# Kernel tuning notes

Measured on AMD Instinct MI355X. Metric: run time of the kernel, lower is better.

The kernel has to match this reference:

```python
import jax, jax.numpy as jnp
import numpy as np

EPS = 1e-7
K = 15      # kernel_size
CIN = 128
F = 256


def setup_inputs() -> dict:
    key = jax.random.key(0)
    k1, k2 = jax.random.split(key)
    x = jax.random.normal(k1, (32, 4096, CIN), dtype=jnp.float32)
    # glorot-uniform init then UnitNorm over axes (0,1) per filter, matching the constraint
    limit = np.sqrt(6.0 / (K * CIN + F))
    kernel = jax.random.uniform(k2, (K, CIN, F), dtype=jnp.float32, minval=-limit, maxval=limit)
    kernel = kernel / jnp.sqrt(jnp.sum(kernel * kernel, axis=(0, 1), keepdims=True) + 1e-12)
    scale = jnp.full((1, 1, 1), 10.0, dtype=jnp.float32)
    bias = jnp.zeros((F,), dtype=jnp.float32)
    return {"inputs": x, "kernel": kernel, "scale": scale, "bias": bias}


def reference(inputs, kernel, scale, bias):
    # dot-product conv: (B, L-K+1, F), VALID padding, stride 1
    dot = jax.lax.conv_general_dilated(
        inputs, kernel, window_strides=(1,), padding="VALID",
        dimension_numbers=("NWC", "WIO", "NWC"))
    # sliding sum-of-squares over window*channels. In the original this is a
    # conv1d with an all-ones (K,CIN,F) kernel, i.e. every filter sees the same
    # scalar sum -> compute it once via a cumsum box filter and broadcast.
    k = kernel.shape[0]
    sq = jnp.sum(inputs * inputs, axis=-1)                       # (B, L)
    cs = jnp.cumsum(jnp.pad(sq, ((0, 0), (1, 0))), axis=1)       # (B, L+1)
    win = cs[:, k:] - cs[:, :-k]                                 # (B, L-K+1)
    norm_x = jnp.sqrt(win + EPS)[..., None]                      # (B, L-K+1, 1)
    return scale * (dot / norm_x) + bias
```

## Files before the change

kernel.cpp:

```cpp
#include <hip/hip_runtime.h>
#include <hip/hip_bf16.h>
#include <stdint.h>

#define K_TAPS 15
#define CIN    128
#define F_OUT  256
#define LSEQ   4096
#define LOUT   (LSEQ - K_TAPS + 1)
#define BATCH  32

typedef __attribute__((ext_vector_type(8))) short bf16x8;
typedef __attribute__((ext_vector_type(4))) float f32x4;

typedef __attribute__((address_space(1))) const unsigned int gu32_t;
typedef __attribute__((address_space(3))) unsigned int su32_t;

__global__ void prep_w_kernel(const float* __restrict__ W,
                              unsigned short* __restrict__ Wp) {
  int idx = blockIdx.x * 256 + threadIdx.x;
  int f  = idx & 255;
  int kc = idx >> 8;
  int c  = kc & 127;
  int k  = kc >> 7;
  float w = W[idx];
  __hip_bfloat16 hb = __float2bfloat16(w);
  int chalf = c >> 6;
  int c6    = c & 63;
  int slot  = ((c6 >> 3) ^ f) & 7;
  int cp    = slot * 8 + (c & 7);
  Wp[((size_t)(k * 2 + chalf) * 256 + f) * 64 + cp] =
      *reinterpret_cast<unsigned short*>(&hb);
}

__global__ void sq_kernel(const float* __restrict__ x, float* __restrict__ sq) {
  int wid  = threadIdx.x >> 6;
  int lane = threadIdx.x & 63;
  int half = lane >> 5;
  int lq   = lane & 31;
  long pos = (long)blockIdx.x * 8 + wid * 2 + half;
  const float4* xp = (const float4*)(x + pos * CIN) + lq;
  float4 v = *xp;
  float s = v.x * v.x + v.y * v.y + v.z * v.z + v.w * v.w;
  #pragma unroll
  for (int m = 1; m <= 16; m <<= 1) s += __shfl_xor(s, m, 64);
  if (lq == 0) sq[pos] = s;
}

__global__ void rn_kernel(const float* __restrict__ sq,
                          const float* __restrict__ scale,
                          float* __restrict__ rn) {
  int t = blockIdx.x * 256 + threadIdx.x;
  int b = blockIdx.y;
  if (t >= LOUT) return;
  const float* s = sq + b * LSEQ + t;
  float w = 0.f;
  #pragma unroll
  for (int k = 0; k < K_TAPS; ++k) w += s[k];
  rn[b * LSEQ + t] = scale[0] / sqrtf(w + 1e-7f);
}

#define BM 256
#define BN 256
#define XROWS 272
#define XBYTES (XROWS * 256)
#define BBYTES 32768
#define NSTEP (K_TAPS * 2)

__global__ __launch_bounds__(512, 2) void conv_gemm_kernel(
    const float* __restrict__ x, const unsigned short* __restrict__ Wp,
    const float* __restrict__ rn, const float* __restrict__ bias,
    float* __restrict__ out)
{
  __shared__ __align__(16) char lds[XBYTES + 2 * BBYTES];
  char* Xs = lds;
  char* Bs = lds + XBYTES;

  const int b  = blockIdx.y;
  const int t0 = blockIdx.x * BM;

  const int tx   = threadIdx.x;
  const int wid  = tx >> 6;
  const int lane = tx & 63;
  const int wm   = wid >> 2;
  const int wn   = wid & 3;

  const int klane = lane >> 4;
  const int rl    = lane & 15;
  const int arow0 = wm * 128;
  const int bcol0 = wn * 64;

  auto stageB = [&](int buf, int step) {
    const char* src = (const char*)Wp + (size_t)step * 32768;
    char* dst = Bs + buf * BBYTES;
    #pragma unroll
    for (int i = 0; i < 4; ++i) {
      int off = i * 8192 + wid * 1024;
      __builtin_amdgcn_global_load_lds(
          (gu32_t*)(src + off + lane * 16),
          (su32_t*)(dst + off), 16, 0, 0);
    }
  };

  stageB(0, 0);

  {
    const int rloc = tx >> 4;
    const int g    = tx & 15;
    const float* xb = x + (long)b * LSEQ * CIN;
    #pragma unroll
    for (int it = 0; it < 9; ++it) {
      int row  = it * 32 + rloc;
      int grow = t0 + row;
      if (row < XROWS) {
        float v[8];
        if (grow < LSEQ) {
          const float4* p = (const float4*)(xb + (long)grow * CIN + g * 8);
          float4 a0 = p[0], a1 = p[1];
          v[0]=a0.x; v[1]=a0.y; v[2]=a0.z; v[3]=a0.w;
          v[4]=a1.x; v[5]=a1.y; v[6]=a1.z; v[7]=a1.w;
        } else {
          #pragma unroll
          for (int j = 0; j < 8; ++j) v[j] = 0.f;
        }
        union { unsigned short us[8]; int4 q; } pk;
        #pragma unroll
        for (int j = 0; j < 8; ++j) {
          __hip_bfloat16 hb = __float2bfloat16(v[j]);
          pk.us[j] = *reinterpret_cast<unsigned short*>(&hb);
        }
        int slot = (g & 8) | ((g ^ row) & 7);
        *(int4*)(Xs + row * 256 + slot * 16) = pk.q;
      }
    }
  }
  __syncthreads();

  f32x4 acc[8][4] = {};

  #pragma unroll 2
  for (int s = 0; s < NSTEP; ++s) {
    const int tap = s >> 1;
    const int ch8 = (s & 1) * 8;
    const char* Bsc = Bs + (s & 1) * BBYTES;

    bf16x8 afA[4], afB[4], bfr0[4], bfr1[4];

    {
      const int ga = ch8 + klane;
      #pragma unroll
      for (int i = 0; i < 4; ++i) {
        int row  = arow0 + i * 16 + rl + tap;
        int slot = (ga & 8) | ((ga ^ row) & 7);
        afA[i] = *(const bf16x8*)(Xs + row * 256 + slot * 16);
      }
      #pragma unroll
      for (int nf = 0; nf < 4; ++nf) {
        int fc   = bcol0 + nf * 16 + rl;
        int slot = (klane ^ fc) & 7;
        bfr0[nf] = *(const bf16x8*)(Bsc + fc * 128 + slot * 16);
      }
      if (s + 1 < NSTEP) stageB((s & 1) ^ 1, s + 1);
    }
    __builtin_amdgcn_s_barrier();
    asm volatile("s_waitcnt lgkmcnt(0)" ::: "memory");
    __builtin_amdgcn_s_setprio(1);
    #pragma unroll
    for (int i = 0; i < 4; ++i)
      #pragma unroll
      for (int nf = 0; nf < 4; ++nf)
        acc[i][nf] = __builtin_amdgcn_mfma_f32_16x16x32_bf16(
            afA[i], bfr0[nf], acc[i][nf], 0, 0, 0);
    __builtin_amdgcn_s_setprio(0);
    __builtin_amdgcn_s_barrier();

    {
      const int ga = ch8 + klane;
      #pragma unroll
      for (int i = 0; i < 4; ++i) {
        int row  = arow0 + (i + 4) * 16 + rl + tap;
        int slot = (ga & 8) | ((ga ^ row) & 7);
        afB[i] = *(const bf16x8*)(Xs + row * 256 + slot * 16);
      }
    }
    __builtin_amdgcn_s_barrier();
    asm volatile("s_waitcnt lgkmcnt(0)" ::: "memory");
    __builtin_amdgcn_s_setprio(1);
    #pragma unroll
    for (int i = 0; i < 4; ++i)
      #pragma unroll
      for (int nf = 0; nf < 4; ++nf)
        acc[i + 4][nf] = __builtin_amdgcn_mfma_f32_16x16x32_bf16(
            afB[i], bfr0[nf], acc[i + 4][nf], 0, 0, 0);
    __builtin_amdgcn_s_setprio(0);
    __builtin_amdgcn_s_barrier();

    {
      const int ga = ch8 + 4 + klane;
      const int gb = 4 + klane;
      #pragma unroll
      for (int i = 0; i < 4; ++i) {
        int row  = arow0 + i * 16 + rl + tap;
        int slot = (ga & 8) | ((ga ^ row) & 7);
        afA[i] = *(const bf16x8*)(Xs + row * 256 + slot * 16);
      }
      #pragma unroll
      for (int nf = 0; nf < 4; ++nf) {
        int fc   = bcol0 + nf * 16 + rl;
        int slot = (gb ^ fc) & 7;
        bfr1[nf] = *(const bf16x8*)(Bsc + fc * 128 + slot * 16);
      }
    }
    __builtin_amdgcn_s_barrier();
    asm volatile("s_waitcnt lgkmcnt(0)" ::: "memory");
    __builtin_amdgcn_s_setprio(1);
    #pragma unroll
    for (int i = 0; i < 4; ++i)
      #pragma unroll
      for (int nf = 0; nf < 4; ++nf)
        acc[i][nf] = __builtin_amdgcn_mfma_f32_16x16x32_bf16(
            afA[i], bfr1[nf], acc[i][nf], 0, 0, 0);
    __builtin_amdgcn_s_setprio(0);
    __builtin_amdgcn_s_barrier();

    {
      const int ga = ch8 + 4 + klane;
      #pragma unroll
      for (int i = 0; i < 4; ++i) {
        int row  = arow0 + (i + 4) * 16 + rl + tap;
        int slot = (ga & 8) | ((ga ^ row) & 7);
        afB[i] = *(const bf16x8*)(Xs + row * 256 + slot * 16);
      }
    }
    __builtin_amdgcn_s_barrier();
    asm volatile("s_waitcnt lgkmcnt(0)" ::: "memory");
    __builtin_amdgcn_s_setprio(1);
    #pragma unroll
    for (int i = 0; i < 4; ++i)
      #pragma unroll
      for (int nf = 0; nf < 4; ++nf)
        acc[i + 4][nf] = __builtin_amdgcn_mfma_f32_16x16x32_bf16(
            afB[i], bfr0 == bfr1 ? bfr1[nf] : bfr1[nf], acc[i + 4][nf], 0, 0, 0);
    __builtin_amdgcn_s_setprio(0);
    asm volatile("s_waitcnt vmcnt(0)" ::: "memory");
    __builtin_amdgcn_s_barrier();
  }

  const int rgrp = lane >> 4;
  float biasv[4];
  #pragma unroll
  for (int nf = 0; nf < 4; ++nf) biasv[nf] = bias[bcol0 + nf * 16 + rl];
  float* ob = out + (long)b * LOUT * F_OUT;
  const float* rnb = rn + b * LSEQ + t0;
  #pragma unroll
  for (int mf = 0; mf < 8; ++mf) {
    #pragma unroll
    for (int r = 0; r < 4; ++r) {
      int row = arow0 + mf * 16 + rgrp * 4 + r;
      int gt  = t0 + row;
      if (gt < LOUT) {
        float rv = rnb[row];
        #pragma unroll
        for (int nf = 0; nf < 4; ++nf) {
          ob[(long)gt * F_OUT + bcol0 + nf * 16 + rl] =
              acc[mf][nf][r] * rv + biasv[nf];
        }
      }
    }
  }
}

extern "C" void kernel_launch(void* const* d_in, const int* in_sizes, int n_in,
                              void* d_out, int out_size, void* d_ws, size_t ws_size,
                              hipStream_t stream) {
  const float* x     = (const float*)d_in[0];
  const float* W     = (const float*)d_in[1];
  const float* scale = (const float*)d_in[2];
  const float* bias  = (const float*)d_in[3];
  float* out = (float*)d_out;

  char* ws = (char*)d_ws;
  unsigned short* Wp = (unsigned short*)ws;
  float* sq = (float*)(ws + 1048576);
  float* rn = (float*)(ws + 1048576 + 524288);

  prep_w_kernel<<<1920, 256, 0, stream>>>(W, Wp);
  sq_kernel<<<BATCH * LSEQ / 8, 256, 0, stream>>>(x, sq);
  rn_kernel<<<dim3((LOUT + 255) / 256, BATCH), 256, 0, stream>>>(sq, scale, rn);
  conv_gemm_kernel<<<dim3(16, BATCH), 512, 0, stream>>>(x, Wp, rn, bias, out);
}
```

Before: 148.1 us.

## Split weight staging into halves with partial vmcnt waits to deepen overlap

Splits each step's weight tile prefetch into two halves, issued at separate points in the loop. Each half is guarded by a partial vmcnt wait before the barrier that precedes its LDS read. This drops the full vmcnt(0) drain at the end of every step, so global-to-LDS loads can stay in flight across MFMA phases. The risk is subtle ordering bugs in the vmcnt counts when the X-tile loads or the final step change the number of loads in flight.

```diff
diff --git a/kernel.cpp b/kernel.cpp
--- a/kernel.cpp
+++ b/kernel.cpp
@@ -89,11 +89,11 @@
   const int arow0 = wm * 128;
   const int bcol0 = wn * 64;
 
-  auto stageB = [&](int buf, int step) {
-    const char* src = (const char*)Wp + (size_t)step * 32768;
-    char* dst = Bs + buf * BBYTES;
-    #pragma unroll
-    for (int i = 0; i < 4; ++i) {
+  auto stageB2 = [&](int buf, int step, int half) {
+    const char* src = (const char*)Wp + (size_t)step * 32768 + half * 16384;
+    char* dst = Bs + buf * BBYTES + half * 16384;
+    #pragma unroll
+    for (int i = 0; i < 2; ++i) {
       int off = i * 8192 + wid * 1024;
       __builtin_amdgcn_global_load_lds(
           (gu32_t*)(src + off + lane * 16),
@@ -101,7 +101,8 @@
     }
   };
 
-  stageB(0, 0);
+  stageB2(0, 0, 0);
+  stageB2(0, 0, 1);
 
   {
     const int rloc = tx >> 4;
@@ -141,7 +142,8 @@
   for (int s = 0; s < NSTEP; ++s) {
     const int tap = s >> 1;
     const int ch8 = (s & 1) * 8;
-    const char* Bsc = Bs + (s & 1) * BBYTES;
+    const int cur = s & 1;
+    const char* Bsc = Bs + cur * BBYTES;
 
     bf16x8 afA[4], afB[4], bfr0[4], bfr1[4];
 
@@ -153,15 +155,22 @@
         int slot = (ga & 8) | ((ga ^ row) & 7);
         afA[i] = *(const bf16x8*)(Xs + row * 256 + slot * 16);
       }
+    }
+    if (s + 1 < NSTEP) {
+      stageB2(cur ^ 1, s + 1, 0);
+      asm volatile("s_waitcnt vmcnt(4)" ::: "memory");
+    } else {
+      asm volatile("s_waitcnt vmcnt(2)" ::: "memory");
+    }
+    __builtin_amdgcn_s_barrier();
+    {
       #pragma unroll
       for (int nf = 0; nf < 4; ++nf) {
         int fc   = bcol0 + nf * 16 + rl;
         int slot = (klane ^ fc) & 7;
         bfr0[nf] = *(const bf16x8*)(Bsc + fc * 128 + slot * 16);
       }
-      if (s + 1 < NSTEP) stageB((s & 1) ^ 1, s + 1);
-    }
-    __builtin_amdgcn_s_barrier();
+    }
     asm volatile("s_waitcnt lgkmcnt(0)" ::: "memory");
     __builtin_amdgcn_s_setprio(1);
     #pragma unroll
@@ -196,13 +205,22 @@
 
     {
       const int ga = ch8 + 4 + klane;
-      const int gb = 4 + klane;
       #pragma unroll
       for (int i = 0; i < 4; ++i) {
         int row  = arow0 + i * 16 + rl + tap;
         int slot = (ga & 8) | ((ga ^ row) & 7);
         afA[i] = *(const bf16x8*)(Xs + row * 256 + slot * 16);
       }
+    }
+    if (s + 1 < NSTEP) {
+      stageB2(cur ^ 1, s + 1, 1);
+      asm volatile("s_waitcnt vmcnt(4)" ::: "memory");
+    } else {
+      asm volatile("s_waitcnt vmcnt(0)" ::: "memory");
+    }
+    __builtin_amdgcn_s_barrier();
+    {
+      const int gb = 4 + klane;
       #pragma unroll
       for (int nf = 0; nf < 4; ++nf) {
         int fc   = bcol0 + nf * 16 + rl;
@@ -210,7 +228,6 @@
         bfr1[nf] = *(const bf16x8*)(Bsc + fc * 128 + slot * 16);
       }
     }
-    __builtin_amdgcn_s_barrier();
     asm volatile("s_waitcnt lgkmcnt(0)" ::: "memory");
     __builtin_amdgcn_s_setprio(1);
     #pragma unroll
@@ -239,9 +256,8 @@
       #pragma unroll
       for (int nf = 0; nf < 4; ++nf)
         acc[i + 4][nf] = __builtin_amdgcn_mfma_f32_16x16x32_bf16(
-            afB[i], bfr0 == bfr1 ? bfr1[nf] : bfr1[nf], acc[i + 4][nf], 0, 0, 0);
+            afB[i], bfr1[nf], acc[i + 4][nf], 0, 0, 0);
     __builtin_amdgcn_s_setprio(0);
-    asm volatile("s_waitcnt vmcnt(0)" ::: "memory");
     __builtin_amdgcn_s_barrier();
   }
 
```

Result: no change. 147.0 us (-0.7%).
